# Performance work log

Hardware: AMD Instinct MI355X
Metric: run time of the kernel (lower is better)

## Reference

```python
import jax, jax.numpy as jnp
import numpy as np

N, F, B, H = 4096, 64, 16, 8  # nodes, feat dim, graphs, GAT heads


def _graph():
    # symmetric random graph (avg deg ~8), plus exact 2-hop and 3-hop edge lists
    # (this reproduces torch_sparse.spspmm with coalesced=True on the boolean structure)
    rng = np.random.default_rng(0)
    s = rng.integers(0, N, 8192)
    d = rng.integers(0, N, 8192)
    m = s != d
    s, d = s[m], d[m]
    rows = np.concatenate([s, d]).astype(np.int64)
    cols = np.concatenate([d, s]).astype(np.int64)
    key = np.unique(rows * N + cols)
    rows, cols = key // N, key % N
    A = np.zeros((N, N), np.float32)
    A[rows, cols] = 1.0
    A2 = (A @ A) > 0
    A3 = (A2.astype(np.float32) @ A) > 0
    np.fill_diagonal(A2, False)  # GATConv/GCNConv remove then re-add self-loops
    np.fill_diagonal(A3, False)
    e1 = np.stack([rows, cols]).astype(np.int64)
    e2 = np.stack(np.nonzero(A2)).astype(np.int64)
    e3 = np.stack(np.nonzero(A3)).astype(np.int64)
    return e1, e2, e3


def _sl(ei, n):
    loops = jnp.arange(n, dtype=ei.dtype)
    return jnp.concatenate([ei, jnp.stack([loops, loops])], axis=1)


def _seg_softmax(logits, seg, n):
    m = jax.ops.segment_max(logits, seg, num_segments=n)
    e = jnp.exp(logits - m[seg])
    s = jax.ops.segment_sum(e, seg, num_segments=n)
    return e / s[seg]


def _gat(x, ei, W, a_src, a_dst, b, heads):
    # PyG GATConv: per-head linear, edge attention logits, softmax over incoming edges
    n = x.shape[0]
    d = a_src.shape[1]
    h = (x @ W).reshape(n, heads, d)  # [N,H,D]
    src, dst = ei[0], ei[1]
    al = jnp.einsum('nhd,hd->nh', h, a_src)
    ar = jnp.einsum('nhd,hd->nh', h, a_dst)
    logit = jax.nn.leaky_relu(al[src] + ar[dst], 0.2)  # [E,H]
    alpha = _seg_softmax(logit, dst, n)
    out = jax.ops.segment_sum(alpha[:, :, None] * h[src], dst, num_segments=n)
    return out.reshape(n, heads * d) + b


def _gcn(x, ei, W, b):
    n = x.shape[0]
    src, dst = ei[0], ei[1]
    h = x @ W
    deg = jax.ops.segment_sum(jnp.ones(src.shape, x.dtype), dst, num_segments=n)
    dinv = jnp.where(deg > 0, deg ** -0.5, 0.0)
    norm = dinv[src] * dinv[dst]
    return jax.ops.segment_sum(norm[:, None] * h[src], dst, num_segments=n) + b


def setup_inputs():
    key = jax.random.key(0)
    ks = iter(jax.random.split(key, 40))
    e1, e2, e3 = _graph()
    p = lambda *shape: jax.random.normal(next(ks), shape, jnp.float32) * 0.1
    return dict(
        x=jax.random.normal(next(ks), (N, F), jnp.float32),
        edge_index=jnp.asarray(e1), edge_index2=jnp.asarray(e2), edge_index3=jnp.asarray(e3),
        batch=jnp.asarray(np.repeat(np.arange(B), N // B)),
        g1_W=p(F, H * F), g1_as=p(H, F), g1_ad=p(H, F), g1_b=p(H * F),
        g2_W=p(H * F, F), g2_as=p(1, F), g2_ad=p(1, F), g2_b=p(F),
        gfc_W=p(F, F), gfc_b=p(F), gfc1_W=p(F, 128), gfc1_b=p(128),
        gout_W=p(128, F), gout_b=p(F),
        c2_W=p(F, 2 * F), c2_b=p(2 * F), c3_W=p(2 * F, 4 * F), c3_b=p(4 * F),
        A_W=p(4 * F, F), A_b=p(F), B_W=p(2 * F, F), B_b=p(F),
        Wih=p(F, 3 * F), Whh=p(F, 3 * F), bih=p(3 * F), bhh=p(3 * F),
        f1_W=p(F, 128), f1_b=p(128), f2_W=p(128, 120), f2_b=p(120),
    )


def reference(x, edge_index, edge_index2, edge_index3, batch,
              g1_W, g1_as, g1_ad, g1_b, g2_W, g2_as, g2_ad, g2_b,
              gfc_W, gfc_b, gfc1_W, gfc1_b, gout_W, gout_b,
              c2_W, c2_b, c3_W, c3_b, A_W, A_b, B_W, B_b,
              Wih, Whh, bih, bhh, f1_W, f1_b, f2_W, f2_b):
    n = x.shape[0]
    e1, e2, e3 = _sl(edge_index, n), _sl(edge_index2, n), _sl(edge_index3, n)

    def gat_block(xin, ei):  # inner GAT module (eval mode: dropouts are identity)
        h = jax.nn.elu(_gat(xin, ei, g1_W, g1_as, g1_ad, g1_b, H))
        h = jax.nn.relu(_gat(h, ei, g2_W, g2_as, g2_ad, g2_b, 1))
        h = jax.nn.relu(h @ gfc_W + gfc_b)
        h = jax.nn.relu(h @ gfc1_W + gfc1_b)
        return h @ gout_W + gout_b

    h1 = jax.nn.relu(gat_block(x, e1))
    h2 = jax.nn.relu(_gcn(h1, e1, c2_W, c2_b))
    h3 = jax.nn.relu(_gcn(h2, e1, c3_W, c3_b))            # [N,4F]
    h4 = jax.nn.relu(gat_block(x, e2))
    h5 = jax.nn.relu(_gcn(h4, e2, c2_W, c2_b))            # [N,2F]
    h6 = jax.nn.relu(gat_block(x, e3))                     # [N,F]

    # GateUpdate
    b_ = h5 @ B_W + B_b
    a_ = h3 @ A_W + A_b
    z = jax.nn.sigmoid(a_ + b_)
    hg = z * b_ + (1 - z) * a_
    # GRUCell(h6, hg)
    gi = h6 @ Wih + bih
    gh = hg @ Whh + bhh
    r = jax.nn.sigmoid(gi[:, :F] + gh[:, :F])
    zz = jax.nn.sigmoid(gi[:, F:2 * F] + gh[:, F:2 * F])
    nn_ = jnp.tanh(gi[:, 2 * F:] + r * gh[:, 2 * F:])
    cc = (1 - zz) * nn_ + zz * hg

    g = jax.ops.segment_max(cc, batch, num_segments=B)    # global_max_pool -> [B,F]
    g = jax.nn.relu(g @ f1_W + f1_b)
    return g @ f2_W + f2_b                                 # [B,120]
```

## Files before the change

### kernel.cpp

```cpp
#include <hip/hip_runtime.h>
#include <math.h>

#define NN 4096
#define NG 16

__global__ void rowptr3_kernel(const int* __restrict__ ea, int Ea,
                               const int* __restrict__ eb, int Eb,
                               const int* __restrict__ ec, int Ec,
                               int* __restrict__ rpa, int* __restrict__ rpb, int* __restrict__ rpc){
    int t = blockIdx.x * blockDim.x + threadIdx.x;
    int set = t / (NN + 1), i = t % (NN + 1);
    if (set >= 3) return;
    const int* e0 = set == 0 ? ea : set == 1 ? eb : ec;
    int E        = set == 0 ? Ea : set == 1 ? Eb : Ec;
    int* rp      = set == 0 ? rpa : set == 1 ? rpb : rpc;
    if (i == NN){ rp[NN] = E; return; }
    int lo = 0, hi = E;
    while (lo < hi){ int mid = (lo + hi) >> 1; if (e0[mid] < i) lo = mid + 1; else hi = mid; }
    rp[i] = lo;
}

__global__ void dinv2_kernel(const int* __restrict__ rp1, const int* __restrict__ rp2,
                             float* __restrict__ dinv1, float* __restrict__ dinv2){
    int t = blockIdx.x * blockDim.x + threadIdx.x;
    int set = t >> 12, i = t & (NN - 1);
    if (set >= 2) return;
    const int* rp = set ? rp2 : rp1;
    float deg = (float)(rp[i+1] - rp[i] + 1);
    (set ? dinv2 : dinv1)[i] = 1.0f / sqrtf(deg);
}

__global__ __launch_bounds__(256)
void gemm_kernel(const float* __restrict__ A, const float* __restrict__ W,
                 const float* __restrict__ bias, float* __restrict__ C,
                 int K, int Nc, int act){
    __shared__ float As[64][17];
    __shared__ float Bs[16][64];
    const int tid = threadIdx.x;
    const int tx = tid & 15, ty = tid >> 4;
    const int row0 = blockIdx.y * 64, col0 = blockIdx.x * 64;
    float acc[4][4] = {};
    for (int k0 = 0; k0 < K; k0 += 16){
        {   int idx = tid * 4; int r = idx >> 4, kk = idx & 15;
            float4 av = *reinterpret_cast<const float4*>(&A[(size_t)(row0 + r) * K + k0 + kk]);
            As[r][kk+0]=av.x; As[r][kk+1]=av.y; As[r][kk+2]=av.z; As[r][kk+3]=av.w; }
        {   int idx = tid * 4; int r = idx >> 6, cc = idx & 63;
            float4 wv = *reinterpret_cast<const float4*>(&W[(size_t)(k0 + r) * Nc + col0 + cc]);
            *reinterpret_cast<float4*>(&Bs[r][cc]) = wv; }
        __syncthreads();
        #pragma unroll
        for (int kk = 0; kk < 16; ++kk){
            float a[4], b[4];
            #pragma unroll
            for (int i = 0; i < 4; ++i) a[i] = As[ty*4+i][kk];
            #pragma unroll
            for (int j = 0; j < 4; ++j) b[j] = Bs[kk][tx*4+j];
            #pragma unroll
            for (int i = 0; i < 4; ++i)
                #pragma unroll
                for (int j = 0; j < 4; ++j) acc[i][j] += a[i]*b[j];
        }
        __syncthreads();
    }
    #pragma unroll
    for (int i = 0; i < 4; ++i){
        int r = row0 + ty*4 + i;
        #pragma unroll
        for (int j = 0; j < 4; ++j){
            int c = col0 + tx*4 + j;
            float v = acc[i][j] + (bias ? bias[c] : 0.0f);
            if (act == 1) v = fmaxf(v, 0.0f);
            C[(size_t)r * Nc + c] = v;
        }
    }
}

__global__ __launch_bounds__(256)
void gemm32_kernel(const float* __restrict__ A, const float* __restrict__ W,
                   const float* __restrict__ bias, float* __restrict__ C,
                   int K, int Nc, int act){
    __shared__ float As[32][17];
    __shared__ float Bs[16][64];
    const int tid = threadIdx.x;
    const int tx = tid & 15, ty = tid >> 4;
    const int row0 = blockIdx.y * 32, col0 = blockIdx.x * 64;
    float acc[2][4] = {};
    for (int k0 = 0; k0 < K; k0 += 16){
        {   int idx = tid * 2; int r = idx >> 4, kk = idx & 15;
            float2 av = *reinterpret_cast<const float2*>(&A[(size_t)(row0 + r) * K + k0 + kk]);
            As[r][kk] = av.x; As[r][kk+1] = av.y; }
        {   int idx = tid * 4; int r = idx >> 6, cc = idx & 63;
            *reinterpret_cast<float4*>(&Bs[r][cc]) =
                *reinterpret_cast<const float4*>(&W[(size_t)(k0 + r) * Nc + col0 + cc]); }
        __syncthreads();
        #pragma unroll
        for (int kk = 0; kk < 16; ++kk){
            float a0 = As[ty*2][kk], a1 = As[ty*2+1][kk];
            float b[4];
            #pragma unroll
            for (int j = 0; j < 4; ++j) b[j] = Bs[kk][tx*4+j];
            #pragma unroll
            for (int j = 0; j < 4; ++j){ acc[0][j] += a0*b[j]; acc[1][j] += a1*b[j]; }
        }
        __syncthreads();
    }
    #pragma unroll
    for (int i = 0; i < 2; ++i){
        int r = row0 + ty*2 + i;
        #pragma unroll
        for (int j = 0; j < 4; ++j){
            int c = col0 + tx*4 + j;
            float v = acc[i][j] + (bias ? bias[c] : 0.0f);
            if (act == 1) v = fmaxf(v, 0.0f);
            C[(size_t)r * Nc + c] = v;
        }
    }
}

template<int NHEADS>
__global__ void attn_dot_kernel(const float* __restrict__ h,
                                const float* __restrict__ a_src, const float* __restrict__ a_dst,
                                float* __restrict__ al, float* __restrict__ ar){
    const int n = blockIdx.x, lane = threadIdx.x;
    for (int hh = 0; hh < NHEADS; ++hh){
        float v = h[(size_t)n * (NHEADS*64) + hh*64 + lane];
        float x = v * a_src[hh*64 + lane];
        float y = v * a_dst[hh*64 + lane];
        #pragma unroll
        for (int off = 1; off < 64; off <<= 1){ x += __shfl_xor(x, off); y += __shfl_xor(y, off); }
        if (lane == 0){ al[n*NHEADS + hh] = x; ar[n*NHEADS + hh] = y; }
    }
}

__global__ __launch_bounds__(64)
void gat_agg8_wave_kernel(const float* __restrict__ hfeat,
                          const float* __restrict__ al, const float* __restrict__ ar,
                          const int* __restrict__ rpA, const int* __restrict__ rpB, const int* __restrict__ rpC,
                          const int* __restrict__ clA, const int* __restrict__ clB, const int* __restrict__ clC,
                          const float* __restrict__ bias, float* __restrict__ out){
    const int bid = blockIdx.x;
    const int set = bid >> 12, i = bid & (NN - 1);
    const int lane = threadIdx.x;
    const int* rowptr = set == 0 ? rpA : set == 1 ? rpB : rpC;
    const int* cols   = set == 0 ? clA : set == 1 ? clB : clC;
    const int start = rowptr[i], end = rowptr[i+1];
    const int deg = end - start;

    float al_i[8], ar_i[8];
    {
        float4 t0 = *reinterpret_cast<const float4*>(&al[(size_t)i*8]);
        float4 t1 = *reinterpret_cast<const float4*>(&al[(size_t)i*8+4]);
        al_i[0]=t0.x; al_i[1]=t0.y; al_i[2]=t0.z; al_i[3]=t0.w;
        al_i[4]=t1.x; al_i[5]=t1.y; al_i[6]=t1.z; al_i[7]=t1.w;
        float4 u0 = *reinterpret_cast<const float4*>(&ar[(size_t)i*8]);
        float4 u1 = *reinterpret_cast<const float4*>(&ar[(size_t)i*8+4]);
        ar_i[0]=u0.x; ar_i[1]=u0.y; ar_i[2]=u0.z; ar_i[3]=u0.w;
        ar_i[4]=u1.x; ar_i[5]=u1.y; ar_i[6]=u1.z; ar_i[7]=u1.w;
    }

    float m[8], s[8];
    #pragma unroll
    for (int h = 0; h < 8; ++h){ m[h] = -1e30f; s[h] = 0.f; }
    for (int k = start + lane; k < end; k += 64){
        int j = cols[k];
        float4 t0 = *reinterpret_cast<const float4*>(&al[(size_t)j*8]);
        float4 t1 = *reinterpret_cast<const float4*>(&al[(size_t)j*8+4]);
        float av[8] = {t0.x,t0.y,t0.z,t0.w,t1.x,t1.y,t1.z,t1.w};
        #pragma unroll
        for (int h = 0; h < 8; ++h){
            float x = av[h] + ar_i[h];
            x = x >= 0.f ? x : 0.2f * x;
            float mn = fmaxf(m[h], x);
            s[h] = s[h] * __expf(m[h] - mn) + __expf(x - mn);
            m[h] = mn;
        }
    }
    if (lane == 0){
        #pragma unroll
        for (int h = 0; h < 8; ++h){
            float x = al_i[h] + ar_i[h];
            x = x >= 0.f ? x : 0.2f * x;
            float mn = fmaxf(m[h], x);
            s[h] = s[h] * __expf(m[h] - mn) + __expf(x - mn);
            m[h] = mn;
        }
    }
    #pragma unroll
    for (int off = 1; off < 64; off <<= 1){
        #pragma unroll
        for (int h = 0; h < 8; ++h){
            float m2 = __shfl_xor(m[h], off), s2 = __shfl_xor(s[h], off);
            float mn = fmaxf(m[h], m2);
            s[h] = s[h] * __expf(m[h] - mn) + s2 * __expf(m2 - mn);
            m[h] = mn;
        }
    }

    __shared__ int   sbuf[64];
    __shared__ float wbuf[64][9];
    const int c0 = 4*lane, c1 = 256 + 4*lane;
    const int h0 = lane >> 4, h1 = 4 + h0;
    float4 A0 = {0.f,0.f,0.f,0.f}, A1 = {0.f,0.f,0.f,0.f};
    for (int k0 = 0; k0 < deg; k0 += 64){
        int cnt = min(64, deg - k0);
        if (lane < cnt) sbuf[lane] = cols[start + k0 + lane];
        __syncthreads();
        if (lane < cnt){
            int j = sbuf[lane];
            float4 t0 = *reinterpret_cast<const float4*>(&al[(size_t)j*8]);
            float4 t1 = *reinterpret_cast<const float4*>(&al[(size_t)j*8+4]);
            float av[8] = {t0.x,t0.y,t0.z,t0.w,t1.x,t1.y,t1.z,t1.w};
            #pragma unroll
            for (int h = 0; h < 8; ++h){
                float x = av[h] + ar_i[h];
                x = x >= 0.f ? x : 0.2f * x;
                wbuf[lane][h] = __expf(x - m[h]);
            }
        }
        __syncthreads();
        int e = 0;
        for (; e + 4 <= cnt; e += 4){
            int j0 = sbuf[e], j1 = sbuf[e+1], j2 = sbuf[e+2], j3 = sbuf[e+3];
            const float* q0 = &hfeat[(size_t)j0*512];
            const float* q1 = &hfeat[(size_t)j1*512];
            const float* q2 = &hfeat[(size_t)j2*512];
            const float* q3 = &hfeat[(size_t)j3*512];
            float4 v00 = *reinterpret_cast<const float4*>(q0 + c0);
            float4 v01 = *reinterpret_cast<const float4*>(q0 + c1);
            float4 v10 = *reinterpret_cast<const float4*>(q1 + c0);
            float4 v11 = *reinterpret_cast<const float4*>(q1 + c1);
            float4 v20 = *reinterpret_cast<const float4*>(q2 + c0);
            float4 v21 = *reinterpret_cast<const float4*>(q2 + c1);
            float4 v30 = *reinterpret_cast<const float4*>(q3 + c0);
            float4 v31 = *reinterpret_cast<const float4*>(q3 + c1);
            float w00 = wbuf[e  ][h0], w01 = wbuf[e  ][h1];
            float w10 = wbuf[e+1][h0], w11 = wbuf[e+1][h1];
            float w20 = wbuf[e+2][h0], w21 = wbuf[e+2][h1];
            float w30 = wbuf[e+3][h0], w31 = wbuf[e+3][h1];
            A0.x += w00*v00.x; A0.y += w00*v00.y; A0.z += w00*v00.z; A0.w += w00*v00.w;
            A1.x += w01*v01.x; A1.y += w01*v01.y; A1.z += w01*v01.z; A1.w += w01*v01.w;
            A0.x += w10*v10.x; A0.y += w10*v10.y; A0.z += w10*v10.z; A0.w += w10*v10.w;
            A1.x += w11*v11.x; A1.y += w11*v11.y; A1.z += w11*v11.z; A1.w += w11*v11.w;
            A0.x += w20*v20.x; A0.y += w20*v20.y; A0.z += w20*v20.z; A0.w += w20*v20.w;
            A1.x += w21*v21.x; A1.y += w21*v21.y; A1.z += w21*v21.z; A1.w += w21*v21.w;
            A0.x += w30*v30.x; A0.y += w30*v30.y; A0.z += w30*v30.z; A0.w += w30*v30.w;
            A1.x += w31*v31.x; A1.y += w31*v31.y; A1.z += w31*v31.z; A1.w += w31*v31.w;
        }
        for (; e < cnt; ++e){
            int j = sbuf[e];
            const float* hp = &hfeat[(size_t)j*512];
            float w0 = wbuf[e][h0], w1 = wbuf[e][h1];
            float4 v0 = *reinterpret_cast<const float4*>(hp + c0);
            float4 v1 = *reinterpret_cast<const float4*>(hp + c1);
            A0.x += w0*v0.x; A0.y += w0*v0.y; A0.z += w0*v0.z; A0.w += w0*v0.w;
            A1.x += w1*v1.x; A1.y += w1*v1.y; A1.z += w1*v1.z; A1.w += w1*v1.w;
        }
        __syncthreads();
    }
    {
        float x0 = al_i[h0] + ar_i[h0]; x0 = x0 >= 0.f ? x0 : 0.2f*x0;
        float x1 = al_i[h1] + ar_i[h1]; x1 = x1 >= 0.f ? x1 : 0.2f*x1;
        float w0 = __expf(x0 - m[h0]), w1 = __expf(x1 - m[h1]);
        float4 hv0 = *reinterpret_cast<const float4*>(&hfeat[(size_t)i*512 + c0]);
        float4 hv1 = *reinterpret_cast<const float4*>(&hfeat[(size_t)i*512 + c1]);
        A0.x += w0*hv0.x; A0.y += w0*hv0.y; A0.z += w0*hv0.z; A0.w += w0*hv0.w;
        A1.x += w1*hv1.x; A1.y += w1*hv1.y; A1.z += w1*hv1.z; A1.w += w1*hv1.w;
        float inv0 = 1.f / s[h0], inv1 = 1.f / s[h1];
        float4 b0 = *reinterpret_cast<const float4*>(&bias[c0]);
        float4 b1 = *reinterpret_cast<const float4*>(&bias[c1]);
        float4 o0, o1;
        o0.x = A0.x*inv0 + b0.x; o0.y = A0.y*inv0 + b0.y;
        o0.z = A0.z*inv0 + b0.z; o0.w = A0.w*inv0 + b0.w;
        o1.x = A1.x*inv1 + b1.x; o1.y = A1.y*inv1 + b1.y;
        o1.z = A1.z*inv1 + b1.z; o1.w = A1.w*inv1 + b1.w;
        o0.x = o0.x > 0.f ? o0.x : __expf(o0.x) - 1.f;
        o0.y = o0.y > 0.f ? o0.y : __expf(o0.y) - 1.f;
        o0.z = o0.z > 0.f ? o0.z : __expf(o0.z) - 1.f;
        o0.w = o0.w > 0.f ? o0.w : __expf(o0.w) - 1.f;
        o1.x = o1.x > 0.f ? o1.x : __expf(o1.x) - 1.f;
        o1.y = o1.y > 0.f ? o1.y : __expf(o1.y) - 1.f;
        o1.z = o1.z > 0.f ? o1.z : __expf(o1.z) - 1.f;
        o1.w = o1.w > 0.f ? o1.w : __expf(o1.w) - 1.f;
        *reinterpret_cast<float4*>(&out[(size_t)bid*512 + c0]) = o0;
        *reinterpret_cast<float4*>(&out[(size_t)bid*512 + c1]) = o1;
    }
}

template<int BLOCK, int NHEADS>
__global__ __launch_bounds__(BLOCK)
void gat_agg_kernel(const float* __restrict__ hfeat,
                    const float* __restrict__ al, const float* __restrict__ ar,
                    const int* __restrict__ rpA, const int* __restrict__ rpB, const int* __restrict__ rpC,
                    const int* __restrict__ clA, const int* __restrict__ clB, const int* __restrict__ clC,
                    const float* __restrict__ bias, float* __restrict__ out,
                    int act, int sharedfeat){
    constexpr int TD    = NHEADS * 64;
    constexpr int CHUNK = BLOCK / NHEADS;
    const int bid = blockIdx.x;
    const int set = bid >> 12, i = bid & (NN - 1);
    const int tid = threadIdx.x;
    const int* rowptr = set == 0 ? rpA : set == 1 ? rpB : rpC;
    const int* cols   = set == 0 ? clA : set == 1 ? clB : clC;
    const int base = sharedfeat ? 0 : set * NN;
    const int start = rowptr[i], end = rowptr[i+1];

    float al_i[NHEADS], ar_i[NHEADS];
    #pragma unroll
    for (int h = 0; h < NHEADS; ++h){
        al_i[h] = al[(size_t)(base + i)*NHEADS + h];
        ar_i[h] = ar[(size_t)(base + i)*NHEADS + h];
    }
    float m[NHEADS], s[NHEADS];
    #pragma unroll
    for (int h = 0; h < NHEADS; ++h){ m[h] = -1e30f; s[h] = 0.f; }
    for (int k = start + tid; k < end; k += BLOCK){
        int j = cols[k];
        #pragma unroll
        for (int h = 0; h < NHEADS; ++h){
            float x = al[(size_t)(base + j)*NHEADS + h] + ar_i[h];
            x = x >= 0.f ? x : 0.2f * x;
            float mn = fmaxf(m[h], x);
            s[h] = s[h] * __expf(m[h] - mn) + __expf(x - mn);
            m[h] = mn;
        }
    }
    if (tid == 0){
        #pragma unroll
        for (int h = 0; h < NHEADS; ++h){
            float x = al_i[h] + ar_i[h];
            x = x >= 0.f ? x : 0.2f * x;
            float mn = fmaxf(m[h], x);
            s[h] = s[h] * __expf(m[h] - mn) + __expf(x - mn);
            m[h] = mn;
        }
    }
    #pragma unroll
    for (int off = 1; off < 64; off <<= 1){
        #pragma unroll
        for (int h = 0; h < NHEADS; ++h){
            float m2 = __shfl_xor(m[h], off), s2 = __shfl_xor(s[h], off);
            float mn = fmaxf(m[h], m2);
            s[h] = s[h] * __expf(m[h] - mn) + s2 * __expf(m2 - mn);
            m[h] = mn;
        }
    }

    __shared__ int   sbuf[CHUNK];
    __shared__ float wbuf[CHUNK][NHEADS];
    const int deg = end - start;
    float p0 = 0.f, p1 = 0.f, p2 = 0.f, p3 = 0.f;
    for (int k0 = 0; k0 < deg; k0 += CHUNK){
        int cnt = min(CHUNK, deg - k0);
        if (tid < cnt) sbuf[tid] = cols[start + k0 + tid];
        __syncthreads();
        if (tid < cnt){
            float x = al[(size_t)(base + sbuf[tid])*NHEADS] + ar_i[0];
            x = x >= 0.f ? x : 0.2f * x;
            wbuf[tid][0] = __expf(x - m[0]);
        }
        __syncthreads();
        int e = 0;
        for (; e + 8 <= cnt; e += 8){
            int j0 = sbuf[e],   j1 = sbuf[e+1], j2 = sbuf[e+2], j3 = sbuf[e+3];
            int j4 = sbuf[e+4], j5 = sbuf[e+5], j6 = sbuf[e+6], j7 = sbuf[e+7];
            float v0 = hfeat[(size_t)(base + j0)*TD + tid];
            float v1 = hfeat[(size_t)(base + j1)*TD + tid];
            float v2 = hfeat[(size_t)(base + j2)*TD + tid];
            float v3 = hfeat[(size_t)(base + j3)*TD + tid];
            float v4 = hfeat[(size_t)(base + j4)*TD + tid];
            float v5 = hfeat[(size_t)(base + j5)*TD + tid];
            float v6 = hfeat[(size_t)(base + j6)*TD + tid];
            float v7 = hfeat[(size_t)(base + j7)*TD + tid];
            p0 += wbuf[e  ][0] * v0; p1 += wbuf[e+1][0] * v1;
            p2 += wbuf[e+2][0] * v2; p3 += wbuf[e+3][0] * v3;
            p0 += wbuf[e+4][0] * v4; p1 += wbuf[e+5][0] * v5;
            p2 += wbuf[e+6][0] * v6; p3 += wbuf[e+7][0] * v7;
        }
        for (; e < cnt; ++e)
            p0 += wbuf[e][0] * hfeat[(size_t)(base + sbuf[e])*TD + tid];
        __syncthreads();
    }
    float acc = (p0 + p1) + (p2 + p3);
    float x = al_i[0] + ar_i[0];
    x = x >= 0.f ? x : 0.2f * x;
    acc += __expf(x - m[0]) * hfeat[(size_t)(base + i)*TD + tid];
    float v = acc / s[0] + bias[tid];
    if (act == 1) v = fmaxf(v, 0.f);
    else          v = v > 0.f ? v : __expf(v) - 1.f;
    out[(size_t)bid*TD + tid] = v;
}

template<int DIM>
__global__ __launch_bounds__(DIM)
void gcn_agg_kernel(const float* __restrict__ h,
                    const int* __restrict__ rpA, const int* __restrict__ rpB,
                    const int* __restrict__ clA, const int* __restrict__ clB,
                    const float* __restrict__ dvA, const float* __restrict__ dvB,
                    const float* __restrict__ bias, float* __restrict__ out){
    const int bid = blockIdx.x;
    const int set = bid >> 12, i = bid & (NN - 1);
    const int* rowptr = set ? rpB : rpA;
    const int* cols   = set ? clB : clA;
    const float* dinv = set ? dvB : dvA;
    const int c = threadIdx.x;
    const int start = rowptr[i], end = rowptr[i+1];
    const float di = dinv[i];
    const size_t rbase = (size_t)(set * NN) * DIM;
    float self = di * di * h[(size_t)bid * DIM + c];
    float p0 = 0.f, p1 = 0.f, p2 = 0.f, p3 = 0.f;
    int k = start;
    for (; k + 8 <= end; k += 8){
        int j0 = cols[k],   j1 = cols[k+1], j2 = cols[k+2], j3 = cols[k+3];
        int j4 = cols[k+4], j5 = cols[k+5], j6 = cols[k+6], j7 = cols[k+7];
        float v0 = h[rbase + (size_t)j0 * DIM + c];
        float v1 = h[rbase + (size_t)j1 * DIM + c];
        float v2 = h[rbase + (size_t)j2 * DIM + c];
        float v3 = h[rbase + (size_t)j3 * DIM + c];
        float v4 = h[rbase + (size_t)j4 * DIM + c];
        float v5 = h[rbase + (size_t)j5 * DIM + c];
        float v6 = h[rbase + (size_t)j6 * DIM + c];
        float v7 = h[rbase + (size_t)j7 * DIM + c];
        p0 += dinv[j0] * v0; p1 += dinv[j1] * v1;
        p2 += dinv[j2] * v2; p3 += dinv[j3] * v3;
        p0 += dinv[j4] * v4; p1 += dinv[j5] * v5;
        p2 += dinv[j6] * v6; p3 += dinv[j7] * v7;
    }
    for (; k < end; ++k){
        int j = cols[k];
        p0 += dinv[j] * h[rbase + (size_t)j * DIM + c];
    }
    float acc = self + di * ((p0 + p1) + (p2 + p3));
    out[(size_t)bid * DIM + c] = fmaxf(acc + bias[c], 0.f);
}

__global__ void gate_kernel(const float* __restrict__ a_, const float* __restrict__ b_,
                            float* __restrict__ hg, int total){
    int idx = blockIdx.x * blockDim.x + threadIdx.x;
    if (idx < total){
        float a = a_[idx], b = b_[idx];
        float z = 1.f / (1.f + expf(-(a + b)));
        hg[idx] = z * b + (1.f - z) * a;
    }
}

__global__ void gru_kernel(const float* __restrict__ gi, const float* __restrict__ gh,
                           const float* __restrict__ hg, float* __restrict__ cc, int total){
    int idx = blockIdx.x * blockDim.x + threadIdx.x;
    if (idx >= total) return;
    int row = idx >> 6, c = idx & 63;
    float r  = 1.f / (1.f + expf(-(gi[row*192 + c]       + gh[row*192 + c])));
    float zz = 1.f / (1.f + expf(-(gi[row*192 + 64 + c]  + gh[row*192 + 64 + c])));
    float nn = tanhf(gi[row*192 + 128 + c] + r * gh[row*192 + 128 + c]);
    cc[idx] = (1.f - zz) * nn + zz * hg[idx];
}

__global__ __launch_bounds__(256)
void head_kernel(const float* __restrict__ cc,
                 const float* __restrict__ f1_W, const float* __restrict__ f1_b,
                 const float* __restrict__ f2_W, const float* __restrict__ f2_b,
                 float* __restrict__ out){
    const int b = blockIdx.x, tid = threadIdx.x;
    const int c = tid & 63, grp = tid >> 6;
    __shared__ float red4[4][64];
    __shared__ float gmax[64];
    __shared__ float fgs[128];
    const float* base = cc + (size_t)(b * (NN / NG)) * 64;
    float m = -1e30f;
    #pragma unroll 8
    for (int n = grp; n < NN / NG; n += 4) m = fmaxf(m, base[n * 64 + c]);
    red4[grp][c] = m;
    __syncthreads();
    if (tid < 64)
        gmax[tid] = fmaxf(fmaxf(red4[0][tid], red4[1][tid]),
                          fmaxf(red4[2][tid], red4[3][tid]));
    __syncthreads();
    if (tid < 128){
        float acc = 0.f;
        #pragma unroll
        for (int k = 0; k < 64; ++k) acc += gmax[k] * f1_W[k * 128 + tid];
        fgs[tid] = fmaxf(acc + f1_b[tid], 0.f);
    }
    __syncthreads();
    if (tid < 120){
        float acc = 0.f;
        #pragma unroll
        for (int k = 0; k < 128; ++k) acc += fgs[k] * f2_W[k * 120 + tid];
        out[b * 120 + tid] = acc + f2_b[tid];
    }
}

extern "C" void kernel_launch(void* const* d_in, const int* in_sizes, int n_in,
                              void* d_out, int out_size, void* d_ws, size_t ws_size,
                              hipStream_t stream){
    const float* x  = (const float*)d_in[0];
    const int* e1 = (const int*)d_in[1]; const int E1 = in_sizes[1] / 2;
    const int* e2 = (const int*)d_in[2]; const int E2 = in_sizes[2] / 2;
    const int* e3 = (const int*)d_in[3]; const int E3 = in_sizes[3] / 2;
    const float* g1_W  = (const float*)d_in[5];
    const float* g1_as = (const float*)d_in[6];
    const float* g1_ad = (const float*)d_in[7];
    const float* g1_b  = (const float*)d_in[8];
    const float* g2_W  = (const float*)d_in[9];
    const float* g2_as = (const float*)d_in[10];
    const float* g2_ad = (const float*)d_in[11];
    const float* g2_b  = (const float*)d_in[12];
    const float* gfc_W = (const float*)d_in[13];
    const float* gfc_b = (const float*)d_in[14];
    const float* gfc1_W= (const float*)d_in[15];
    const float* gfc1_b= (const float*)d_in[16];
    const float* gout_W= (const float*)d_in[17];
    const float* gout_b= (const float*)d_in[18];
    const float* c2_W  = (const float*)d_in[19];
    const float* c2_b  = (const float*)d_in[20];
    const float* c3_W  = (const float*)d_in[21];
    const float* c3_b  = (const float*)d_in[22];
    const float* A_W   = (const float*)d_in[23];
    const float* A_b   = (const float*)d_in[24];
    const float* B_W   = (const float*)d_in[25];
    const float* B_b   = (const float*)d_in[26];
    const float* Wih   = (const float*)d_in[27];
    const float* Whh   = (const float*)d_in[28];
    const float* bih   = (const float*)d_in[29];
    const float* bhh   = (const float*)d_in[30];
    const float* f1_W  = (const float*)d_in[31];
    const float* f1_b  = (const float*)d_in[32];
    const float* f2_W  = (const float*)d_in[33];
    const float* f2_b  = (const float*)d_in[34];
    float* out = (float*)d_out;

    int* ip = (int*)d_ws;
    int* rp1 = ip; int* rp2 = ip + 4100; int* rp3 = ip + 8200;
    float* fb = (float*)(ip + 12300);
    size_t o = 0;
    auto alloc = [&](size_t nf){ float* p = fb + o; o += nf; return p; };
    float* dinv1 = alloc(NN);
    float* dinv2 = alloc(NN);
    float* hbuf  = alloc((size_t)NN*512);
    float* al1   = alloc((size_t)NN*8);
    float* ar1   = alloc((size_t)NN*8);
    float* bigA  = alloc((size_t)3*NN*512);
    float* t2    = alloc((size_t)3*NN*64);
    float* al2   = alloc((size_t)3*NN);
    float* ar2   = alloc((size_t)3*NN);
    (void)ws_size; (void)n_in; (void)out_size;

    float* eluo3 = bigA;
    float* g2o   = bigA;
    float* fc1   = bigA + (size_t)786432;
    float* fc2   = bigA + (size_t)1572864;
    float* houts = hbuf;
    float* h1    = houts;
    float* h6    = houts + (size_t)2*NN*64;
    float* gcnx2 = bigA + (size_t)3145728;
    float* h25   = bigA + (size_t)4194304;
    float* h2    = h25;
    float* h5    = h25 + (size_t)NN*128;
    float* gcnx3 = bigA;
    float* h3    = bigA + (size_t)1048576;
    float* a_    = bigA + (size_t)2097152;
    float* b_    = bigA + (size_t)2359296;
    float* hg    = bigA + (size_t)2621440;
    float* gi    = bigA + (size_t)2883584;
    float* gh    = bigA + (size_t)3670016;
    float* ccb   = bigA + (size_t)4456448;
    const int* cols1 = e1 + E1; const int* cols2 = e2 + E2; const int* cols3 = e3 + E3;

    rowptr3_kernel<<<(3*(NN+1)+255)/256, 256, 0, stream>>>(e1, E1, e2, E2, e3, E3, rp1, rp2, rp3);
    dinv2_kernel<<<2*NN/256, 256, 0, stream>>>(rp1, rp2, dinv1, dinv2);

    gemm_kernel<<<dim3(8, 64), 256, 0, stream>>>(x, g1_W, nullptr, hbuf, 64, 512, 0);
    attn_dot_kernel<8><<<NN, 64, 0, stream>>>(hbuf, g1_as, g1_ad, al1, ar1);
    gat_agg8_wave_kernel<<<3*NN, 64, 0, stream>>>(hbuf, al1, ar1,
        rp1, rp2, rp3, cols1, cols2, cols3, g1_b, eluo3);
    gemm32_kernel<<<dim3(1, 384), 256, 0, stream>>>(eluo3, g2_W, nullptr, t2, 512, 64, 0);
    attn_dot_kernel<1><<<3*NN, 64, 0, stream>>>(t2, g2_as, g2_ad, al2, ar2);
    gat_agg_kernel<64,1><<<3*NN, 64, 0, stream>>>(t2, al2, ar2,
        rp1, rp2, rp3, cols1, cols2, cols3, g2_b, g2o, 1, 0);
    gemm32_kernel<<<dim3(1, 384), 256, 0, stream>>>(g2o, gfc_W, gfc_b, fc1, 64, 64, 1);
    gemm_kernel<<<dim3(2, 192), 256, 0, stream>>>(fc1, gfc1_W, gfc1_b, fc2, 64, 128, 1);
    gemm32_kernel<<<dim3(1, 384), 256, 0, stream>>>(fc2, gout_W, gout_b, houts, 128, 64, 1);

    gemm_kernel<<<dim3(2, 128), 256, 0, stream>>>(houts, c2_W, nullptr, gcnx2, 64, 128, 0);
    gcn_agg_kernel<128><<<2*NN, 128, 0, stream>>>(gcnx2, rp1, rp2, cols1, cols2,
                                                  dinv1, dinv2, c2_b, h25);
    gemm_kernel<<<dim3(4, 64), 256, 0, stream>>>(h2, c3_W, nullptr, gcnx3, 128, 256, 0);
    gcn_agg_kernel<256><<<NN, 256, 0, stream>>>(gcnx3, rp1, rp1, cols1, cols1,
                                                dinv1, dinv1, c3_b, h3);

    gemm32_kernel<<<dim3(1, 128), 256, 0, stream>>>(h3, A_W, A_b, a_, 256, 64, 0);
    gemm32_kernel<<<dim3(1, 128), 256, 0, stream>>>(h5, B_W, B_b, b_, 128, 64, 0);
    gate_kernel<<<NN*64/256, 256, 0, stream>>>(a_, b_, hg, NN*64);
    gemm32_kernel<<<dim3(3, 128), 256, 0, stream>>>(h6, Wih, bih, gi, 64, 192, 0);
    gemm32_kernel<<<dim3(3, 128), 256, 0, stream>>>(hg, Whh, bhh, gh, 64, 192, 0);
    gru_kernel<<<NN*64/256, 256, 0, stream>>>(gi, gh, hg, ccb, NN*64);

    head_kernel<<<NG, 256, 0, stream>>>(ccb, f1_W, f1_b, f2_W, f2_b, out);
}
```

Baseline: 387.7 us.

## Pack four waves per GAT block and fuse FC chain into one kernel

The GAT aggregation kernels now run four independent 64-lane waves per 256-thread block, each with private shared buffers and wave barriers instead of block-wide __syncthreads. The single-head GAT aggregation gets a dedicated wave kernel. The three post-GAT fully connected layers (64->64->128->64 with ReLU) are fused into one persistent kernel that keeps two weight matrices in shared memory and processes rows per wave, avoiding two intermediate global buffers and two launches. Buffer offsets are adjusted so the GCN scratch no longer overlaps the relocated data. The fused FC kernel does scalar per-row matvecs, which may use less parallelism than the tiled GEMMs it replaces.

```diff
diff --git a/kernel.cpp b/kernel.cpp
--- a/kernel.cpp
+++ b/kernel.cpp
@@ -3,6 +3,7 @@
 
 #define NN 4096
 #define NG 16
+#define WB() __builtin_amdgcn_wave_barrier()
 
 __global__ void rowptr3_kernel(const int* __restrict__ ea, int Ea,
                                const int* __restrict__ eb, int Eb,
@@ -132,15 +133,15 @@
     }
 }
 
-__global__ __launch_bounds__(64)
+__global__ __launch_bounds__(256)
 void gat_agg8_wave_kernel(const float* __restrict__ hfeat,
                           const float* __restrict__ al, const float* __restrict__ ar,
                           const int* __restrict__ rpA, const int* __restrict__ rpB, const int* __restrict__ rpC,
                           const int* __restrict__ clA, const int* __restrict__ clB, const int* __restrict__ clC,
                           const float* __restrict__ bias, float* __restrict__ out){
-    const int bid = blockIdx.x;
-    const int set = bid >> 12, i = bid & (NN - 1);
-    const int lane = threadIdx.x;
+    const int lane = threadIdx.x & 63, wid = threadIdx.x >> 6;
+    const int g = blockIdx.x * 4 + wid;
+    const int set = g >> 12, i = g & (NN - 1);
     const int* rowptr = set == 0 ? rpA : set == 1 ? rpB : rpC;
     const int* cols   = set == 0 ? clA : set == 1 ? clB : clC;
     const int start = rowptr[i], end = rowptr[i+1];
@@ -196,17 +197,17 @@
         }
     }
 
-    __shared__ int   sbuf[64];
-    __shared__ float wbuf[64][9];
+    __shared__ int   sb[4][64];
+    __shared__ float wb[4][64][9];
     const int c0 = 4*lane, c1 = 256 + 4*lane;
     const int h0 = lane >> 4, h1 = 4 + h0;
     float4 A0 = {0.f,0.f,0.f,0.f}, A1 = {0.f,0.f,0.f,0.f};
     for (int k0 = 0; k0 < deg; k0 += 64){
         int cnt = min(64, deg - k0);
-        if (lane < cnt) sbuf[lane] = cols[start + k0 + lane];
-        __syncthreads();
+        WB();
         if (lane < cnt){
-            int j = sbuf[lane];
+            int j = cols[start + k0 + lane];
+            sb[wid][lane] = j;
             float4 t0 = *reinterpret_cast<const float4*>(&al[(size_t)j*8]);
             float4 t1 = *reinterpret_cast<const float4*>(&al[(size_t)j*8+4]);
             float av[8] = {t0.x,t0.y,t0.z,t0.w,t1.x,t1.y,t1.z,t1.w};
@@ -214,13 +215,13 @@
             for (int h = 0; h < 8; ++h){
                 float x = av[h] + ar_i[h];
                 x = x >= 0.f ? x : 0.2f * x;
-                wbuf[lane][h] = __expf(x - m[h]);
+                wb[wid][lane][h] = __expf(x - m[h]);
             }
         }
-        __syncthreads();
+        WB();
         int e = 0;
         for (; e + 4 <= cnt; e += 4){
-            int j0 = sbuf[e], j1 = sbuf[e+1], j2 = sbuf[e+2], j3 = sbuf[e+3];
+            int j0 = sb[wid][e], j1 = sb[wid][e+1], j2 = sb[wid][e+2], j3 = sb[wid][e+3];
             const float* q0 = &hfeat[(size_t)j0*512];
             const float* q1 = &hfeat[(size_t)j1*512];
             const float* q2 = &hfeat[(size_t)j2*512];
@@ -233,10 +234,10 @@
             float4 v21 = *reinterpret_cast<const float4*>(q2 + c1);
             float4 v30 = *reinterpret_cast<const float4*>(q3 + c0);
             float4 v31 = *reinterpret_cast<const float4*>(q3 + c1);
-            float w00 = wbuf[e  ][h0], w01 = wbuf[e  ][h1];
-            float w10 = wbuf[e+1][h0], w11 = wbuf[e+1][h1];
-            float w20 = wbuf[e+2][h0], w21 = wbuf[e+2][h1];
-            float w30 = wbuf[e+3][h0], w31 = wbuf[e+3][h1];
+            float w00 = wb[wid][e  ][h0], w01 = wb[wid][e  ][h1];
+            float w10 = wb[wid][e+1][h0], w11 = wb[wid][e+1][h1];
+            float w20 = wb[wid][e+2][h0], w21 = wb[wid][e+2][h1];
+            float w30 = wb[wid][e+3][h0], w31 = wb[wid][e+3][h1];
             A0.x += w00*v00.x; A0.y += w00*v00.y; A0.z += w00*v00.z; A0.w += w00*v00.w;
             A1.x += w01*v01.x; A1.y += w01*v01.y; A1.z += w01*v01.z; A1.w += w01*v01.w;
             A0.x += w10*v10.x; A0.y += w10*v10.y; A0.z += w10*v10.z; A0.w += w10*v10.w;
@@ -247,15 +248,14 @@
             A1.x += w31*v31.x; A1.y += w31*v31.y; A1.z += w31*v31.z; A1.w += w31*v31.w;
         }
         for (; e < cnt; ++e){
-            int j = sbuf[e];
+            int j = sb[wid][e];
             const float* hp = &hfeat[(size_t)j*512];
-            float w0 = wbuf[e][h0], w1 = wbuf[e][h1];
+            float w0 = wb[wid][e][h0], w1 = wb[wid][e][h1];
             float4 v0 = *reinterpret_cast<const float4*>(hp + c0);
             float4 v1 = *reinterpret_cast<const float4*>(hp + c1);
             A0.x += w0*v0.x; A0.y += w0*v0.y; A0.z += w0*v0.z; A0.w += w0*v0.w;
             A1.x += w1*v1.x; A1.y += w1*v1.y; A1.z += w1*v1.z; A1.w += w1*v1.w;
         }
-        __syncthreads();
     }
     {
         float x0 = al_i[h0] + ar_i[h0]; x0 = x0 >= 0.f ? x0 : 0.2f*x0;
@@ -281,113 +281,144 @@
         o1.y = o1.y > 0.f ? o1.y : __expf(o1.y) - 1.f;
         o1.z = o1.z > 0.f ? o1.z : __expf(o1.z) - 1.f;
         o1.w = o1.w > 0.f ? o1.w : __expf(o1.w) - 1.f;
-        *reinterpret_cast<float4*>(&out[(size_t)bid*512 + c0]) = o0;
-        *reinterpret_cast<float4*>(&out[(size_t)bid*512 + c1]) = o1;
-    }
-}
-
-template<int BLOCK, int NHEADS>
-__global__ __launch_bounds__(BLOCK)
-void gat_agg_kernel(const float* __restrict__ hfeat,
-                    const float* __restrict__ al, const float* __restrict__ ar,
-                    const int* __restrict__ rpA, const int* __restrict__ rpB, const int* __restrict__ rpC,
-                    const int* __restrict__ clA, const int* __restrict__ clB, const int* __restrict__ clC,
-                    const float* __restrict__ bias, float* __restrict__ out,
-                    int act, int sharedfeat){
-    constexpr int TD    = NHEADS * 64;
-    constexpr int CHUNK = BLOCK / NHEADS;
-    const int bid = blockIdx.x;
-    const int set = bid >> 12, i = bid & (NN - 1);
-    const int tid = threadIdx.x;
+        *reinterpret_cast<float4*>(&out[(size_t)g*512 + c0]) = o0;
+        *reinterpret_cast<float4*>(&out[(size_t)g*512 + c1]) = o1;
+    }
+}
+
+__global__ __launch_bounds__(256)
+void gat_agg1_wave_kernel(const float* __restrict__ hfeat,
+                          const float* __restrict__ al, const float* __restrict__ ar,
+                          const int* __restrict__ rpA, const int* __restrict__ rpB, const int* __restrict__ rpC,
+                          const int* __restrict__ clA, const int* __restrict__ clB, const int* __restrict__ clC,
+                          const float* __restrict__ bias, float* __restrict__ out){
+    const int lane = threadIdx.x & 63, wid = threadIdx.x >> 6;
+    const int g = blockIdx.x * 4 + wid;
+    const int set = g >> 12, i = g & (NN - 1);
     const int* rowptr = set == 0 ? rpA : set == 1 ? rpB : rpC;
     const int* cols   = set == 0 ? clA : set == 1 ? clB : clC;
-    const int base = sharedfeat ? 0 : set * NN;
+    const int base = set * NN;
     const int start = rowptr[i], end = rowptr[i+1];
-
-    float al_i[NHEADS], ar_i[NHEADS];
-    #pragma unroll
-    for (int h = 0; h < NHEADS; ++h){
-        al_i[h] = al[(size_t)(base + i)*NHEADS + h];
-        ar_i[h] = ar[(size_t)(base + i)*NHEADS + h];
-    }
-    float m[NHEADS], s[NHEADS];
-    #pragma unroll
-    for (int h = 0; h < NHEADS; ++h){ m[h] = -1e30f; s[h] = 0.f; }
-    for (int k = start + tid; k < end; k += BLOCK){
+    const int deg = end - start;
+
+    const float al_i = al[(size_t)base + i];
+    const float ar_i = ar[(size_t)base + i];
+
+    float m = -1e30f, s = 0.f;
+    for (int k = start + lane; k < end; k += 64){
         int j = cols[k];
-        #pragma unroll
-        for (int h = 0; h < NHEADS; ++h){
-            float x = al[(size_t)(base + j)*NHEADS + h] + ar_i[h];
-            x = x >= 0.f ? x : 0.2f * x;
-            float mn = fmaxf(m[h], x);
-            s[h] = s[h] * __expf(m[h] - mn) + __expf(x - mn);
-            m[h] = mn;
-        }
-    }
-    if (tid == 0){
-        #pragma unroll
-        for (int h = 0; h < NHEADS; ++h){
-            float x = al_i[h] + ar_i[h];
-            x = x >= 0.f ? x : 0.2f * x;
-            float mn = fmaxf(m[h], x);
-            s[h] = s[h] * __expf(m[h] - mn) + __expf(x - mn);
-            m[h] = mn;
-        }
+        float x = al[(size_t)base + j] + ar_i;
+        x = x >= 0.f ? x : 0.2f * x;
+        float mn = fmaxf(m, x);
+        s = s * __expf(m - mn) + __expf(x - mn);
+        m = mn;
+    }
+    if (lane == 0){
+        float x = al_i + ar_i;
+        x = x >= 0.f ? x : 0.2f * x;
+        float mn = fmaxf(m, x);
+        s = s * __expf(m - mn) + __expf(x - mn);
+        m = mn;
     }
     #pragma unroll
     for (int off = 1; off < 64; off <<= 1){
-        #pragma unroll
-        for (int h = 0; h < NHEADS; ++h){
-            float m2 = __shfl_xor(m[h], off), s2 = __shfl_xor(s[h], off);
-            float mn = fmaxf(m[h], m2);
-            s[h] = s[h] * __expf(m[h] - mn) + s2 * __expf(m2 - mn);
-            m[h] = mn;
-        }
-    }
-
-    __shared__ int   sbuf[CHUNK];
-    __shared__ float wbuf[CHUNK][NHEADS];
-    const int deg = end - start;
+        float m2 = __shfl_xor(m, off), s2 = __shfl_xor(s, off);
+        float mn = fmaxf(m, m2);
+        s = s * __expf(m - mn) + s2 * __expf(m2 - mn);
+        m = mn;
+    }
+
+    __shared__ int   sb[4][64];
+    __shared__ float wbv[4][64];
     float p0 = 0.f, p1 = 0.f, p2 = 0.f, p3 = 0.f;
-    for (int k0 = 0; k0 < deg; k0 += CHUNK){
-        int cnt = min(CHUNK, deg - k0);
-        if (tid < cnt) sbuf[tid] = cols[start + k0 + tid];
-        __syncthreads();
-        if (tid < cnt){
-            float x = al[(size_t)(base + sbuf[tid])*NHEADS] + ar_i[0];
+    for (int k0 = 0; k0 < deg; k0 += 64){
+        int cnt = min(64, deg - k0);
+        WB();
+        if (lane < cnt){
+            int j = cols[start + k0 + lane];
+            sb[wid][lane] = j;
+            float x = al[(size_t)base + j] + ar_i;
             x = x >= 0.f ? x : 0.2f * x;
-            wbuf[tid][0] = __expf(x - m[0]);
-        }
-        __syncthreads();
+            wbv[wid][lane] = __expf(x - m);
+        }
+        WB();
         int e = 0;
         for (; e + 8 <= cnt; e += 8){
-            int j0 = sbuf[e],   j1 = sbuf[e+1], j2 = sbuf[e+2], j3 = sbuf[e+3];
-            int j4 = sbuf[e+4], j5 = sbuf[e+5], j6 = sbuf[e+6], j7 = sbuf[e+7];
-            float v0 = hfeat[(size_t)(base + j0)*TD + tid];
-            float v1 = hfeat[(size_t)(base + j1)*TD + tid];
-            float v2 = hfeat[(size_t)(base + j2)*TD + tid];
-            float v3 = hfeat[(size_t)(base + j3)*TD + tid];
-            float v4 = hfeat[(size_t)(base + j4)*TD + tid];
-            float v5 = hfeat[(size_t)(base + j5)*TD + tid];
-            float v6 = hfeat[(size_t)(base + j6)*TD + tid];
-            float v7 = hfeat[(size_t)(base + j7)*TD + tid];
-            p0 += wbuf[e  ][0] * v0; p1 += wbuf[e+1][0] * v1;
-            p2 += wbuf[e+2][0] * v2; p3 += wbuf[e+3][0] * v3;
-            p0 += wbuf[e+4][0] * v4; p1 += wbuf[e+5][0] * v5;
-            p2 += wbuf[e+6][0] * v6; p3 += wbuf[e+7][0] * v7;
+            int j0 = sb[wid][e],   j1 = sb[wid][e+1], j2 = sb[wid][e+2], j3 = sb[wid][e+3];
+            int j4 = sb[wid][e+4], j5 = sb[wid][e+5], j6 = sb[wid][e+6], j7 = sb[wid][e+7];
+            float v0 = hfeat[(size_t)(base + j0)*64 + lane];
+            float v1 = hfeat[(size_t)(base + j1)*64 + lane];
+            float v2 = hfeat[(size_t)(base + j2)*64 + lane];
+            float v3 = hfeat[(size_t)(base + j3)*64 + lane];
+            float v4 = hfeat[(size_t)(base + j4)*64 + lane];
+            float v5 = hfeat[(size_t)(base + j5)*64 + lane];
+            float v6 = hfeat[(size_t)(base + j6)*64 + lane];
+            float v7 = hfeat[(size_t)(base + j7)*64 + lane];
+            p0 += wbv[wid][e  ] * v0; p1 += wbv[wid][e+1] * v1;
+            p2 += wbv[wid][e+2] * v2; p3 += wbv[wid][e+3] * v3;
+            p0 += wbv[wid][e+4] * v4; p1 += wbv[wid][e+5] * v5;
+            p2 += wbv[wid][e+6] * v6; p3 += wbv[wid][e+7] * v7;
         }
         for (; e < cnt; ++e)
-            p0 += wbuf[e][0] * hfeat[(size_t)(base + sbuf[e])*TD + tid];
-        __syncthreads();
+            p0 += wbv[wid][e] * hfeat[(size_t)(base + sb[wid][e])*64 + lane];
     }
     float acc = (p0 + p1) + (p2 + p3);
-    float x = al_i[0] + ar_i[0];
+    float x = al_i + ar_i;
     x = x >= 0.f ? x : 0.2f * x;
-    acc += __expf(x - m[0]) * hfeat[(size_t)(base + i)*TD + tid];
-    float v = acc / s[0] + bias[tid];
-    if (act == 1) v = fmaxf(v, 0.f);
-    else          v = v > 0.f ? v : __expf(v) - 1.f;
-    out[(size_t)bid*TD + tid] = v;
+    acc += __expf(x - m) * hfeat[(size_t)(base + i)*64 + lane];
+    float v = acc / s + bias[lane];
+    out[(size_t)g*64 + lane] = fmaxf(v, 0.f);
+}
+
+__global__ __launch_bounds__(256)
+void fc_chain_kernel(const float* __restrict__ g2o,
+                     const float* __restrict__ W1, const float* __restrict__ b1,
+                     const float* __restrict__ W2, const float* __restrict__ b2,
+                     const float* __restrict__ W3, const float* __restrict__ b3,
+                     float* __restrict__ out){
+    __shared__ float W1s[64][64];
+    __shared__ float W2s[64][128];
+    __shared__ float b1s[64], b2s[128], b3s[64];
+    __shared__ float rowb[4][64];
+    __shared__ float f2b[4][128];
+    const int tid = threadIdx.x, lane = tid & 63, wid = tid >> 6;
+    for (int idx = tid; idx < 64*64/4; idx += 256)
+        *reinterpret_cast<float4*>(&W1s[0][0] + idx*4) =
+            *reinterpret_cast<const float4*>(W1 + idx*4);
+    for (int idx = tid; idx < 64*128/4; idx += 256)
+        *reinterpret_cast<float4*>(&W2s[0][0] + idx*4) =
+            *reinterpret_cast<const float4*>(W2 + idx*4);
+    if (tid < 64)  b1s[tid] = b1[tid];
+    if (tid < 128) b2s[tid] = b2[tid];
+    if (tid < 64)  b3s[tid] = b3[tid];
+    __syncthreads();
+
+    for (int r = blockIdx.x * 4 + wid; r < 3*NN; r += gridDim.x * 4){
+        WB();
+        rowb[wid][lane] = g2o[(size_t)r*64 + lane];
+        WB();
+        float a1 = b1s[lane];
+        #pragma unroll 8
+        for (int k = 0; k < 64; ++k) a1 += rowb[wid][k] * W1s[k][lane];
+        a1 = fmaxf(a1, 0.f);
+        WB();
+        rowb[wid][lane] = a1;
+        WB();
+        float a2a = b2s[lane], a2b = b2s[lane + 64];
+        #pragma unroll 8
+        for (int k = 0; k < 64; ++k){
+            float v = rowb[wid][k];
+            a2a += v * W2s[k][lane];
+            a2b += v * W2s[k][lane + 64];
+        }
+        f2b[wid][lane]      = fmaxf(a2a, 0.f);
+        f2b[wid][lane + 64] = fmaxf(a2b, 0.f);
+        WB();
+        float a3 = b3s[lane];
+        #pragma unroll 8
+        for (int k = 0; k < 128; ++k) a3 += f2b[wid][k] * W3[k*64 + lane];
+        out[(size_t)r*64 + lane] = fmaxf(a3, 0.f);
+    }
 }
 
 template<int DIM>
@@ -546,8 +577,6 @@
 
     float* eluo3 = bigA;
     float* g2o   = bigA;
-    float* fc1   = bigA + (size_t)786432;
-    float* fc2   = bigA + (size_t)1572864;
     float* houts = hbuf;
     float* h1    = houts;
     float* h6    = houts + (size_t)2*NN*64;
@@ -555,8 +584,8 @@
     float* h25   = bigA + (size_t)4194304;
     float* h2    = h25;
     float* h5    = h25 + (size_t)NN*128;
-    float* gcnx3 = bigA;
-    float* h3    = bigA + (size_t)1048576;
+    float* gcnx3 = bigA + (size_t)786432;
+    float* h3    = bigA + (size_t)1048576 + (size_t)786432;
     float* a_    = bigA + (size_t)2097152;
     float* b_    = bigA + (size_t)2359296;
     float* hg    = bigA + (size_t)2621440;
@@ -570,15 +599,14 @@
 
     gemm_kernel<<<dim3(8, 64), 256, 0, stream>>>(x, g1_W, nullptr, hbuf, 64, 512, 0);
     attn_dot_kernel<8><<<NN, 64, 0, stream>>>(hbuf, g1_as, g1_ad, al1, ar1);
-    gat_agg8_wave_kernel<<<3*NN, 64, 0, stream>>>(hbuf, al1, ar1,
+    gat_agg8_wave_kernel<<<3*NN/4, 256, 0, stream>>>(hbuf, al1, ar1,
         rp1, rp2, rp3, cols1, cols2, cols3, g1_b, eluo3);
     gemm32_kernel<<<dim3(1, 384), 256, 0, stream>>>(eluo3, g2_W, nullptr, t2, 512, 64, 0);
     attn_dot_kernel<1><<<3*NN, 64, 0, stream>>>(t2, g2_as, g2_ad, al2, ar2);
-    gat_agg_kernel<64,1><<<3*NN, 64, 0, stream>>>(t2, al2, ar2,
-        rp1, rp2, rp3, cols1, cols2, cols3, g2_b, g2o, 1, 0);
-    gemm32_kernel<<<dim3(1, 384), 256, 0, stream>>>(g2o, gfc_W, gfc_b, fc1, 64, 64, 1);
-    gemm_kernel<<<dim3(2, 192), 256, 0, stream>>>(fc1, gfc1_W, gfc1_b, fc2, 64, 128, 1);
-    gemm32_kernel<<<dim3(1, 384), 256, 0, stream>>>(fc2, gout_W, gout_b, houts, 128, 64, 1);
+    gat_agg1_wave_kernel<<<3*NN/4, 256, 0, stream>>>(t2, al2, ar2,
+        rp1, rp2, rp3, cols1, cols2, cols3, g2_b, g2o);
+    fc_chain_kernel<<<768, 256, 0, stream>>>(g2o, gfc_W, gfc_b, gfc1_W, gfc1_b,
+                                             gout_W, gout_b, houts);
 
     gemm_kernel<<<dim3(2, 128), 256, 0, stream>>>(houts, c2_W, nullptr, gcnx2, 64, 128, 0);
     gcn_agg_kernel<128><<<2*NN, 128, 0, stream>>>(gcnx2, rp1, rp2, cols1, cols2,
```

Result: slower. 407.5 us (+5.1%).

## Fuse gate and GRU GEMMs into one per-row kernel; batch attention dots

Applied to the files above, without the earlier changes.

Replaces the four small GEMM launches plus the gate and GRU elementwise kernels with a single kernel. Each wave handles one node row, staging its inputs in shared memory and computing the A/B projections, gate, both GRU projections and the final cell output without global intermediates. The attention-dot kernels now pack four nodes per 256-thread block, and the 8-head version does all head reductions in parallel. This cuts launch count and intermediate global traffic. The fused GEMMs re-read weights per row from cache with no tiling, which could cost more than the tiled GEMMs did.

```diff
diff --git a/kernel.cpp b/kernel.cpp
--- a/kernel.cpp
+++ b/kernel.cpp
@@ -3,6 +3,7 @@
 
 #define NN 4096
 #define NG 16
+#define WB() __builtin_amdgcn_wave_barrier()
 
 __global__ void rowptr3_kernel(const int* __restrict__ ea, int Ea,
                                const int* __restrict__ eb, int Eb,
@@ -117,19 +118,44 @@
     }
 }
 
-template<int NHEADS>
-__global__ void attn_dot_kernel(const float* __restrict__ h,
-                                const float* __restrict__ a_src, const float* __restrict__ a_dst,
-                                float* __restrict__ al, float* __restrict__ ar){
-    const int n = blockIdx.x, lane = threadIdx.x;
-    for (int hh = 0; hh < NHEADS; ++hh){
-        float v = h[(size_t)n * (NHEADS*64) + hh*64 + lane];
-        float x = v * a_src[hh*64 + lane];
-        float y = v * a_dst[hh*64 + lane];
-        #pragma unroll
-        for (int off = 1; off < 64; off <<= 1){ x += __shfl_xor(x, off); y += __shfl_xor(y, off); }
-        if (lane == 0){ al[n*NHEADS + hh] = x; ar[n*NHEADS + hh] = y; }
-    }
+__global__ __launch_bounds__(256)
+void attn_dot8_kernel(const float* __restrict__ h,
+                      const float* __restrict__ a_src, const float* __restrict__ a_dst,
+                      float* __restrict__ al, float* __restrict__ ar){
+    const int lane = threadIdx.x & 63, wid = threadIdx.x >> 6;
+    const int n = blockIdx.x * 4 + wid;
+    float x[8], y[8];
+    #pragma unroll
+    for (int c = 0; c < 8; ++c){
+        float v = h[(size_t)n*512 + c*64 + lane];
+        x[c] = v * a_src[c*64 + lane];
+        y[c] = v * a_dst[c*64 + lane];
+    }
+    #pragma unroll
+    for (int off = 1; off < 64; off <<= 1){
+        #pragma unroll
+        for (int c = 0; c < 8; ++c){
+            x[c] += __shfl_xor(x[c], off);
+            y[c] += __shfl_xor(y[c], off);
+        }
+    }
+    if (lane == 0){
+        #pragma unroll
+        for (int c = 0; c < 8; ++c){ al[n*8 + c] = x[c]; ar[n*8 + c] = y[c]; }
+    }
+}
+
+__global__ __launch_bounds__(256)
+void attn_dot1_kernel(const float* __restrict__ h,
+                      const float* __restrict__ a_src, const float* __restrict__ a_dst,
+                      float* __restrict__ al, float* __restrict__ ar){
+    const int lane = threadIdx.x & 63, wid = threadIdx.x >> 6;
+    const int n = blockIdx.x * 4 + wid;
+    float v = h[(size_t)n*64 + lane];
+    float x = v * a_src[lane], y = v * a_dst[lane];
+    #pragma unroll
+    for (int off = 1; off < 64; off <<= 1){ x += __shfl_xor(x, off); y += __shfl_xor(y, off); }
+    if (lane == 0){ al[n] = x; ar[n] = y; }
 }
 
 __global__ __launch_bounds__(64)
@@ -433,25 +459,50 @@
     out[(size_t)bid * DIM + c] = fmaxf(acc + bias[c], 0.f);
 }
 
-__global__ void gate_kernel(const float* __restrict__ a_, const float* __restrict__ b_,
-                            float* __restrict__ hg, int total){
-    int idx = blockIdx.x * blockDim.x + threadIdx.x;
-    if (idx < total){
-        float a = a_[idx], b = b_[idx];
-        float z = 1.f / (1.f + expf(-(a + b)));
-        hg[idx] = z * b + (1.f - z) * a;
-    }
-}
-
-__global__ void gru_kernel(const float* __restrict__ gi, const float* __restrict__ gh,
-                           const float* __restrict__ hg, float* __restrict__ cc, int total){
-    int idx = blockIdx.x * blockDim.x + threadIdx.x;
-    if (idx >= total) return;
-    int row = idx >> 6, c = idx & 63;
-    float r  = 1.f / (1.f + expf(-(gi[row*192 + c]       + gh[row*192 + c])));
-    float zz = 1.f / (1.f + expf(-(gi[row*192 + 64 + c]  + gh[row*192 + 64 + c])));
-    float nn = tanhf(gi[row*192 + 128 + c] + r * gh[row*192 + 128 + c]);
-    cc[idx] = (1.f - zz) * nn + zz * hg[idx];
+__global__ __launch_bounds__(256)
+void gate_gru_kernel(const float* __restrict__ h3, const float* __restrict__ h5,
+                     const float* __restrict__ h6,
+                     const float* __restrict__ A_W, const float* __restrict__ A_b,
+                     const float* __restrict__ B_W, const float* __restrict__ B_b,
+                     const float* __restrict__ Wih, const float* __restrict__ bih,
+                     const float* __restrict__ Whh, const float* __restrict__ bhh,
+                     float* __restrict__ cc){
+    __shared__ float l3[4][256];
+    __shared__ float l5[4][128];
+    __shared__ float l6[4][64];
+    __shared__ float lhg[4][64];
+    const int lane = threadIdx.x & 63, wid = threadIdx.x >> 6;
+    const int r = blockIdx.x * 4 + wid;
+    for (int c = lane; c < 256; c += 64) l3[wid][c] = h3[(size_t)r*256 + c];
+    for (int c = lane; c < 128; c += 64) l5[wid][c] = h5[(size_t)r*128 + c];
+    l6[wid][lane] = h6[(size_t)r*64 + lane];
+    WB();
+    float a = A_b[lane];
+    #pragma unroll 8
+    for (int k = 0; k < 256; ++k) a += l3[wid][k] * A_W[k*64 + lane];
+    float b = B_b[lane];
+    #pragma unroll 8
+    for (int k = 0; k < 128; ++k) b += l5[wid][k] * B_W[k*64 + lane];
+    float z = 1.f / (1.f + expf(-(a + b)));
+    float hg = z * b + (1.f - z) * a;
+    lhg[wid][lane] = hg;
+    WB();
+    float gi0 = bih[lane], gi1 = bih[64 + lane], gi2 = bih[128 + lane];
+    float gh0 = bhh[lane], gh1 = bhh[64 + lane], gh2 = bhh[128 + lane];
+    #pragma unroll 4
+    for (int k = 0; k < 64; ++k){
+        float v6 = l6[wid][k], vh = lhg[wid][k];
+        gi0 += v6 * Wih[k*192 + lane];
+        gi1 += v6 * Wih[k*192 + 64 + lane];
+        gi2 += v6 * Wih[k*192 + 128 + lane];
+        gh0 += vh * Whh[k*192 + lane];
+        gh1 += vh * Whh[k*192 + 64 + lane];
+        gh2 += vh * Whh[k*192 + 128 + lane];
+    }
+    float rr = 1.f / (1.f + expf(-(gi0 + gh0)));
+    float zz = 1.f / (1.f + expf(-(gi1 + gh1)));
+    float nn = tanhf(gi2 + rr * gh2);
+    cc[(size_t)r*64 + lane] = (1.f - zz) * nn + zz * hg;
 }
 
 __global__ __launch_bounds__(256)
@@ -557,11 +608,6 @@
     float* h5    = h25 + (size_t)NN*128;
     float* gcnx3 = bigA;
     float* h3    = bigA + (size_t)1048576;
-    float* a_    = bigA + (size_t)2097152;
-    float* b_    = bigA + (size_t)2359296;
-    float* hg    = bigA + (size_t)2621440;
-    float* gi    = bigA + (size_t)2883584;
-    float* gh    = bigA + (size_t)3670016;
     float* ccb   = bigA + (size_t)4456448;
     const int* cols1 = e1 + E1; const int* cols2 = e2 + E2; const int* cols3 = e3 + E3;
 
@@ -569,11 +615,11 @@
     dinv2_kernel<<<2*NN/256, 256, 0, stream>>>(rp1, rp2, dinv1, dinv2);
 
     gemm_kernel<<<dim3(8, 64), 256, 0, stream>>>(x, g1_W, nullptr, hbuf, 64, 512, 0);
-    attn_dot_kernel<8><<<NN, 64, 0, stream>>>(hbuf, g1_as, g1_ad, al1, ar1);
+    attn_dot8_kernel<<<NN/4, 256, 0, stream>>>(hbuf, g1_as, g1_ad, al1, ar1);
     gat_agg8_wave_kernel<<<3*NN, 64, 0, stream>>>(hbuf, al1, ar1,
         rp1, rp2, rp3, cols1, cols2, cols3, g1_b, eluo3);
     gemm32_kernel<<<dim3(1, 384), 256, 0, stream>>>(eluo3, g2_W, nullptr, t2, 512, 64, 0);
-    attn_dot_kernel<1><<<3*NN, 64, 0, stream>>>(t2, g2_as, g2_ad, al2, ar2);
+    attn_dot1_kernel<<<3*NN/4, 256, 0, stream>>>(t2, g2_as, g2_ad, al2, ar2);
     gat_agg_kernel<64,1><<<3*NN, 64, 0, stream>>>(t2, al2, ar2,
         rp1, rp2, rp3, cols1, cols2, cols3, g2_b, g2o, 1, 0);
     gemm32_kernel<<<dim3(1, 384), 256, 0, stream>>>(g2o, gfc_W, gfc_b, fc1, 64, 64, 1);
@@ -587,12 +633,8 @@
     gcn_agg_kernel<256><<<NN, 256, 0, stream>>>(gcnx3, rp1, rp1, cols1, cols1,
                                                 dinv1, dinv1, c3_b, h3);
 
-    gemm32_kernel<<<dim3(1, 128), 256, 0, stream>>>(h3, A_W, A_b, a_, 256, 64, 0);
-    gemm32_kernel<<<dim3(1, 128), 256, 0, stream>>>(h5, B_W, B_b, b_, 128, 64, 0);
-    gate_kernel<<<NN*64/256, 256, 0, stream>>>(a_, b_, hg, NN*64);
-    gemm32_kernel<<<dim3(3, 128), 256, 0, stream>>>(h6, Wih, bih, gi, 64, 192, 0);
-    gemm32_kernel<<<dim3(3, 128), 256, 0, stream>>>(hg, Whh, bhh, gh, 64, 192, 0);
-    gru_kernel<<<NN*64/256, 256, 0, stream>>>(gi, gh, hg, ccb, NN*64);
+    gate_gru_kernel<<<NN/4, 256, 0, stream>>>(h3, h5, h6, A_W, A_b, B_W, B_b,
+                                              Wih, bih, Whh, bhh, ccb);
 
     head_kernel<<<NG, 256, 0, stream>>>(ccb, f1_W, f1_b, f2_W, f2_b, out);
 }
```

After: 376.6 us. 1.03x faster.
